# Optimization experiments

Measured on AMD Instinct MI355X. Metric: run time of the kernel, lower is better.

The kernel has to match this reference:

```python
import jax, jax.numpy as jnp
import numpy as np

B, S, E, H = 8, 512, 1024, 16
Dh = E // H
MAX_LEN = 512


def setup_inputs() -> dict:
    key = jax.random.key(0)
    ks = jax.random.split(key, 16)
    std = 1.0 / np.sqrt(E)
    inp = {
        "query": jax.random.normal(ks[0], (B, S, E), jnp.float32),
        "key": jax.random.normal(ks[1], (B, S, E), jnp.float32),
        "value": jax.random.normal(ks[2], (B, S, E), jnp.float32),
        "Wq": jax.random.normal(ks[3], (E, E), jnp.float32) * std,
        "bq": jax.random.normal(ks[4], (E,), jnp.float32) * std,
        "Wk": jax.random.normal(ks[5], (E, E), jnp.float32) * std,
        "bk": jax.random.normal(ks[6], (E,), jnp.float32) * std,
        "Wv": jax.random.normal(ks[7], (E, E), jnp.float32) * std,
        "bv": jax.random.normal(ks[8], (E,), jnp.float32) * std,
        "Wo": jax.random.normal(ks[9], (E, E), jnp.float32) * std,
        "bo": jax.random.normal(ks[10], (E,), jnp.float32) * std,
        "pos": jax.random.normal(ks[11], (MAX_LEN, 1, E), jnp.float32),
    }
    return inp


def reference(query, key, value, Wq, bq, Wk, bk, Wv, bv, Wo, bo, pos):
    b, sq, e = query.shape
    s = min(sq, key.shape[1])  # target_seq_length (static)
    scale = np.sqrt(Dh).astype(np.float32)
    pe = pos[:s, 0, :][None]  # [1, s, E] broadcast over batch
    q = query[:, :s] @ Wq.T + bq + pe
    k = key[:, :s] @ Wk.T + bk + pe
    v = value[:, :s] @ Wv.T + bv + pe
    # [b, s, H, Dh]
    q = q.reshape(b, s, H, Dh)
    k = k.reshape(b, s, H, Dh)
    v = v.reshape(b, s, H, Dh)
    scores = jnp.einsum("bqhd,bkhd->bhqk", q, k) / scale
    attn = jax.nn.softmax(scores, axis=-1)
    wv = jnp.einsum("bhqk,bkhd->bqhd", attn, v).reshape(b, s, e)
    return wv @ Wo.T + bo
```

## Files before the change

### kernel.cpp

```cpp
#include <hip/hip_runtime.h>
#include <hip/hip_bf16.h>

typedef __attribute__((ext_vector_type(8))) short bfx8;
typedef __attribute__((ext_vector_type(4))) short bfx4;
typedef __attribute__((ext_vector_type(4))) float fx4;

static __device__ __forceinline__ short f2bf(float f) {
  union { float f; unsigned u; } v; v.f = f;
  unsigned r = v.u + 0x7fffu + ((v.u >> 16) & 1u);
  return (short)(r >> 16);
}

static __device__ __forceinline__ void gld16(const void* g, void* l) {
  __builtin_amdgcn_global_load_lds(
      (const __attribute__((address_space(1))) void*)g,
      (__attribute__((address_space(3))) void*)l, 16, 0, 0);
}

constexpr int Bz = 8, Sq = 512, Em = 1024, Hn = 16, Dh = 64;
constexpr int Mrows = Bz * Sq;
constexpr size_t NE = (size_t)Mrows * Em;
constexpr size_t WE = (size_t)Em * Em;
constexpr int NT = Em / 64;

__global__ __launch_bounds__(256) void convert_kernel(
    const float* __restrict__ q, const float* __restrict__ k,
    const float* __restrict__ v,
    const float* __restrict__ Wq, const float* __restrict__ Wk,
    const float* __restrict__ Wv, const float* __restrict__ Wo,
    short* __restrict__ qx, short* __restrict__ kx, short* __restrict__ vx,
    short* __restrict__ wqb, short* __restrict__ wkb,
    short* __restrict__ wvb, short* __restrict__ wob)
{
  const size_t c = (size_t)blockIdx.x * 256 + threadIdx.x;
  constexpr size_t CI = NE / 8;
  constexpr size_t CW = WE / 8;
  const float* src; short* dst; size_t off;
  if (c < 3 * CI) {
    const int sgi = (int)(c / CI);
    src = sgi == 0 ? q : sgi == 1 ? k : v;
    dst = sgi == 0 ? qx : sgi == 1 ? kx : vx;
    off = (c - (size_t)sgi * CI) * 8;
  } else {
    const size_t w = c - 3 * CI;
    const int sgi = (int)(w / CW);
    src = sgi == 0 ? Wq : sgi == 1 ? Wk : sgi == 2 ? Wv : Wo;
    dst = sgi == 0 ? wqb : sgi == 1 ? wkb : sgi == 2 ? wvb : wob;
    off = (w - (size_t)sgi * CW) * 8;
  }
  fx4 a = *(const fx4*)(src + off);
  fx4 b = *(const fx4*)(src + off + 4);
  bfx8 o = { f2bf(a[0]), f2bf(a[1]), f2bf(a[2]), f2bf(a[3]),
             f2bf(b[0]), f2bf(b[1]), f2bf(b[2]), f2bf(b[3]) };
  *(bfx8*)(dst + off) = o;
}

__global__ __launch_bounds__(512, 2) void gemm_qkv_bf16(
    const short* __restrict__ qx, const short* __restrict__ kx,
    const short* __restrict__ vx,
    const short* __restrict__ Wqb, const short* __restrict__ Wkb,
    const short* __restrict__ Wvb,
    const float* __restrict__ bq, const float* __restrict__ bk,
    const float* __restrict__ bv,
    const float* __restrict__ pos,
    short* __restrict__ qb, short* __restrict__ kb, short* __restrict__ vb)
{
  __shared__ short SM[65536];

  const int z = blockIdx.z;
  const short* X = (z == 0) ? qx : (z == 1) ? kx : vx;
  const short* W = (z == 0) ? Wqb : (z == 1) ? Wkb : Wvb;
  const float* bias = (z == 0) ? bq : (z == 1) ? bk : bv;
  short* dst = (z == 0) ? qb : (z == 1) ? kb : vb;

  const int t0b = blockIdx.x * 256;
  const int f0 = blockIdx.y * 256;
  const int t = threadIdx.x, lane = t & 63, wave = t >> 6;
  const int wr = wave >> 2;
  const int wn = wave & 3;
  const int fr = lane & 15, fq = lane >> 4;

  const int srow = t >> 3;
  const int scc = (t & 7) ^ (srow & 7);
  const int sdst = wave * 512;

  const int sw0 = (fq ^ (fr & 7)) * 8;
  const int sw1 = ((4 + fq) ^ (fr & 7)) * 8;

  auto stageA = [&](int hh, int ktn, int pn) {
    const short* s = W + (size_t)(f0 + hh * 128 + srow) * Em + ktn * 64 + scc * 8;
    short* d = SM + pn * 32768 + hh * 8192 + sdst;
    gld16(s, d);
    gld16(s + (size_t)64 * Em, d + 4096);
  };
  auto stageB = [&](int hh, int ktn, int pn) {
    const short* s = X + (size_t)(t0b + hh * 128 + srow) * Em + ktn * 64 + scc * 8;
    short* d = SM + pn * 32768 + 16384 + hh * 8192 + sdst;
    gld16(s, d);
    gld16(s + (size_t)64 * Em, d + 4096);
  };

  fx4 acc[8][4] = {};

  stageA(0, 0, 0); stageA(1, 0, 0); stageB(0, 0, 0); stageB(1, 0, 0);
  __builtin_amdgcn_sched_barrier(0);
  asm volatile("s_waitcnt vmcnt(0)");
  __builtin_amdgcn_sched_barrier(0);
  __builtin_amdgcn_s_barrier();

  for (int kt = 0; kt < NT; ++kt) {
    const int p = kt & 1, pn = p ^ 1;
    const bool pre = (kt + 1 < NT);
    const short* Ab = SM + p * 32768 + wr * 8192;
    const short* Bb = SM + p * 32768 + 16384 + (wn >> 1) * 8192 + (wn & 1) * 4096;

    bfx8 bf[4][2];
#pragma unroll
    for (int q = 0; q < 4; ++q) {
      if (q == 0) {
#pragma unroll
        for (int cg = 0; cg < 4; ++cg) {
          bf[cg][0] = *(const bfx8*)&Bb[(cg * 16 + fr) * 64 + sw0];
          bf[cg][1] = *(const bfx8*)&Bb[(cg * 16 + fr) * 64 + sw1];
        }
      }
      bfx8 af[2][2];
#pragma unroll
      for (int rr2 = 0; rr2 < 2; ++rr2) {
        const int row = (q * 2 + rr2) * 16 + fr;
        af[rr2][0] = *(const bfx8*)&Ab[row * 64 + sw0];
        af[rr2][1] = *(const bfx8*)&Ab[row * 64 + sw1];
      }
      if (q == 0 && pre) { stageA(0, kt + 1, pn); stageA(1, kt + 1, pn); }
      if (q == 1 && pre) { stageB(0, kt + 1, pn); stageB(1, kt + 1, pn); }

      __builtin_amdgcn_sched_barrier(0);
      __builtin_amdgcn_s_barrier();
      __builtin_amdgcn_sched_barrier(0);

      __builtin_amdgcn_s_setprio(1);
#pragma unroll
      for (int rr2 = 0; rr2 < 2; ++rr2)
#pragma unroll
        for (int cg = 0; cg < 4; ++cg) {
          acc[q * 2 + rr2][cg] = __builtin_amdgcn_mfma_f32_16x16x32_bf16(
              af[rr2][0], bf[cg][0], acc[q * 2 + rr2][cg], 0, 0, 0);
          acc[q * 2 + rr2][cg] = __builtin_amdgcn_mfma_f32_16x16x32_bf16(
              af[rr2][1], bf[cg][1], acc[q * 2 + rr2][cg], 0, 0, 0);
        }
      __builtin_amdgcn_s_setprio(0);
      __builtin_amdgcn_sched_barrier(0);

      if (q == 3 && pre) {
        asm volatile("s_waitcnt vmcnt(0)");
        __builtin_amdgcn_sched_barrier(0);
      }
      __builtin_amdgcn_s_barrier();
    }
  }

  const int b = t0b >> 9;
  if (z < 2) {
#pragma unroll
    for (int fp = 0; fp < 2; ++fp) {
      if (fp) __syncthreads();
      if (wr == fp) {
#pragma unroll
        for (int rg = 0; rg < 8; ++rg) {
          const int nloc = rg * 16 + fq * 4;
          const int nng = f0 + fp * 128 + nloc;
          const fx4 bb = *(const fx4*)&bias[nng];
#pragma unroll
          for (int cg = 0; cg < 4; ++cg) {
            const int token = wn * 64 + cg * 16 + fr;
            const int s = (t0b + token) & (Sq - 1);
            const fx4 pe = *(const fx4*)&pos[(size_t)s * Em + nng];
            const fx4 a = acc[rg][cg];
            bfx4 o = { f2bf(a[0] + bb[0] + pe[0]), f2bf(a[1] + bb[1] + pe[1]),
                       f2bf(a[2] + bb[2] + pe[2]), f2bf(a[3] + bb[3] + pe[3]) };
            *(bfx4*)&SM[token * 136 + nloc] = o;
          }
        }
      }
      __syncthreads();
#pragma unroll
      for (int it = 0; it < 8; ++it) {
        const int flat = it * 512 + t;
        const int token = flat >> 4, ch = flat & 15;
        bfx8 val = *(const bfx8*)&SM[token * 136 + ch * 8];
        const int nng = f0 + fp * 128 + ch * 8;
        const int h = nng >> 6, d = nng & 63;
        const int s = (t0b + token) & (Sq - 1);
        *(bfx8*)&dst[(((size_t)b * Hn + h) * Sq + s) * Dh + d] = val;
      }
    }
  } else {
#pragma unroll
    for (int fp = 0; fp < 2; ++fp) {
      if (fp) __syncthreads();
      if (wr == fp) {
#pragma unroll
        for (int rg = 0; rg < 8; ++rg) {
          const int nloc = rg * 16 + fq * 4;
          const int nng = f0 + fp * 128 + nloc;
          const fx4 bb = *(const fx4*)&bias[nng];
#pragma unroll
          for (int cg = 0; cg < 4; ++cg) {
            const int token = wn * 64 + cg * 16 + fr;
            const int s = (t0b + token) & (Sq - 1);
            const fx4 pe = *(const fx4*)&pos[(size_t)s * Em + nng];
            const fx4 a = acc[rg][cg];
#pragma unroll
            for (int i = 0; i < 4; ++i)
              SM[(nloc + i) * 264 + token] = f2bf(a[i] + bb[i] + pe[i]);
          }
        }
      }
      __syncthreads();
      const int s0 = t0b & (Sq - 1);
#pragma unroll
      for (int it = 0; it < 8; ++it) {
        const int flat = it * 512 + t;
        const int row = flat >> 5, ch = flat & 31;
        bfx8 val = *(const bfx8*)&SM[row * 264 + ch * 8];
        const int nng = f0 + fp * 128 + row;
        const int h = nng >> 6, d = nng & 63;
        *(bfx8*)&dst[(((size_t)b * Hn + h) * Dh + d) * Sq + s0 + ch * 8] = val;
      }
    }
  }
}

constexpr int LDP = 136;

__global__ __launch_bounds__(256, 4) void gemm_out_bf16(
    const short* __restrict__ wv, const short* __restrict__ Wob,
    const float* __restrict__ bo, float* __restrict__ out)
{
  __shared__ short SMo[2 * 8192];
  short* As = SMo;
  short* Bs = SMo + 8192;

  const int m0 = blockIdx.x * 128;
  const int n0 = blockIdx.y * 128;
  const int t = threadIdx.x, lane = t & 63, wave = t >> 6;
  const int wr = wave >> 1, wc = wave & 1;
  const int fr = lane & 15, fq = lane >> 4;

  const int trow = t >> 3;
  const int scol = ((t & 7) ^ (trow & 7)) * 8;
  const short* gW = Wob + (size_t)(n0 + trow) * Em + scol;
  const short* gX = wv + (size_t)(m0 + trow) * Em + scol;
  short* lA = As + wave * 512;
  short* lB = Bs + wave * 512;

  const int sw0 = ((fq ^ (fr & 7)) * 8);
  const int sw1 = (((4 + fq) ^ (fr & 7)) * 8);

  fx4 acc[4][4] = {};

  for (int k0 = 0; k0 < Em; k0 += 64) {
#pragma unroll
    for (int r = 0; r < 4; ++r) {
      gld16(gW + (size_t)(32 * r) * Em + k0, lA + r * 2048);
      gld16(gX + (size_t)(32 * r) * Em + k0, lB + r * 2048);
    }
    __syncthreads();

#pragma unroll
    for (int ks = 0; ks < 2; ++ks) {
      const int sw = ks ? sw1 : sw0;
      bfx8 af[4], bf[4];
#pragma unroll
      for (int u = 0; u < 4; ++u)
        af[u] = *(const bfx8*)&As[(wr * 64 + u * 16 + fr) * 64 + sw];
#pragma unroll
      for (int v = 0; v < 4; ++v)
        bf[v] = *(const bfx8*)&Bs[(wc * 64 + v * 16 + fr) * 64 + sw];
#pragma unroll
      for (int u = 0; u < 4; ++u)
#pragma unroll
        for (int v = 0; v < 4; ++v)
          acc[u][v] = __builtin_amdgcn_mfma_f32_16x16x32_bf16(af[u], bf[v], acc[u][v], 0, 0, 0);
    }
    __syncthreads();
  }

#pragma unroll
  for (int u = 0; u < 4; ++u) {
    const int nn = n0 + wr * 64 + u * 16 + fq * 4;
    const fx4 bb = *(const fx4*)&bo[nn];
#pragma unroll
    for (int v = 0; v < 4; ++v) {
      const int m = m0 + wc * 64 + v * 16 + fr;
      fx4 val = acc[u][v];
      val[0] += bb[0]; val[1] += bb[1]; val[2] += bb[2]; val[3] += bb[3];
      *(fx4*)&out[(size_t)m * Em + nn] = val;
    }
  }
}

constexpr int KVB = 64, LDK = 72;

__global__ __launch_bounds__(512) void attn_kernel(
    const short* __restrict__ qb, const short* __restrict__ kb,
    const short* __restrict__ vb, short* __restrict__ wv)
{
  __shared__ short Ks[KVB * LDK];
  __shared__ short Vt[Dh * LDK];
  __shared__ short Ps[8][16 * LDK];

  const int bh = blockIdx.x;
  const int qt = blockIdx.y;
  const int t = threadIdx.x, lane = t & 63, wave = t >> 6;
  const int fr = lane & 15, fq = lane >> 4;

  const size_t base = (size_t)bh * Sq * Dh;
  const int q0 = qt * 128 + wave * 16;

  bfx8 qf[2];
  {
    const short* qp = qb + base + (size_t)(q0 + fr) * Dh;
    qf[0] = *(const bfx8*)(qp + fq * 8);
    qf[1] = *(const bfx8*)(qp + 32 + fq * 8);
  }

  const int kr = t >> 3, kc = (t & 7) * 8;
  const short* kbp = kb + base + (size_t)kr * Dh + kc;
  const short* vbp = vb + base + (size_t)kr * Sq + kc;

  {
    bfx8 k0 = *(const bfx8*)kbp;
    bfx8 v0 = *(const bfx8*)vbp;
    *(bfx8*)&Ks[kr * LDK + kc] = k0;
    *(bfx8*)&Vt[kr * LDK + kc] = v0;
  }
  __syncthreads();

  float mrow[4] = { -1e30f, -1e30f, -1e30f, -1e30f };
  float lrow[4] = { 0.f, 0.f, 0.f, 0.f };
  fx4 oacc[4] = {};

  for (int kv0 = 0; kv0 < Sq; kv0 += KVB) {
    const bool more = (kv0 + KVB) < Sq;
    bfx8 nk0, nv0;
    if (more) {
      nk0 = *(const bfx8*)(kbp + (size_t)(kv0 + KVB) * Dh);
      nv0 = *(const bfx8*)(vbp + kv0 + KVB);
    }

    fx4 sa[4] = {};
    __builtin_amdgcn_s_setprio(1);
#pragma unroll
    for (int nf = 0; nf < 4; ++nf) {
#pragma unroll
      for (int ks = 0; ks < 2; ++ks) {
        bfx8 kf = *(const bfx8*)&Ks[(nf * 16 + fr) * LDK + ks * 32 + fq * 8];
        sa[nf] = __builtin_amdgcn_mfma_f32_16x16x32_bf16(qf[ks], kf, sa[nf], 0, 0, 0);
      }
    }
    __builtin_amdgcn_s_setprio(0);

#pragma unroll
    for (int i = 0; i < 4; ++i) {
      float mx = fmaxf(fmaxf(sa[0][i], sa[1][i]), fmaxf(sa[2][i], sa[3][i]));
      mx = fmaxf(mx, __shfl_xor(mx, 1));
      mx = fmaxf(mx, __shfl_xor(mx, 2));
      mx = fmaxf(mx, __shfl_xor(mx, 4));
      mx = fmaxf(mx, __shfl_xor(mx, 8));
      mx *= 0.125f;
      if (mx > mrow[i] + 8.f) {
        const float alpha = __expf(mrow[i] - mx);
        mrow[i] = mx;
        lrow[i] *= alpha;
#pragma unroll
        for (int df = 0; df < 4; ++df) oacc[df][i] *= alpha;
      }
      float rs = 0.f;
#pragma unroll
      for (int nf = 0; nf < 4; ++nf) {
        const float p = __expf(sa[nf][i] * 0.125f - mrow[i]);
        rs += p;
        Ps[wave][(fq * 4 + i) * LDK + nf * 16 + fr] = f2bf(p);
      }
      rs += __shfl_xor(rs, 1);
      rs += __shfl_xor(rs, 2);
      rs += __shfl_xor(rs, 4);
      rs += __shfl_xor(rs, 8);
      lrow[i] += rs;
    }

    bfx8 pf[2];
    pf[0] = *(const bfx8*)&Ps[wave][fr * LDK + fq * 8];
    pf[1] = *(const bfx8*)&Ps[wave][fr * LDK + 32 + fq * 8];
    __builtin_amdgcn_s_setprio(1);
#pragma unroll
    for (int df = 0; df < 4; ++df) {
#pragma unroll
      for (int ks = 0; ks < 2; ++ks) {
        bfx8 vf = *(const bfx8*)&Vt[(df * 16 + fr) * LDK + ks * 32 + fq * 8];
        oacc[df] = __builtin_amdgcn_mfma_f32_16x16x32_bf16(pf[ks], vf, oacc[df], 0, 0, 0);
      }
    }
    __builtin_amdgcn_s_setprio(0);
    __syncthreads();

    if (more) {
      *(bfx8*)&Ks[kr * LDK + kc] = nk0;
      *(bfx8*)&Vt[kr * LDK + kc] = nv0;
      __syncthreads();
    }
  }

  const int b = bh >> 4, h = bh & 15;
#pragma unroll
  for (int df = 0; df < 4; ++df) {
    const int d = df * 16 + fr;
#pragma unroll
    for (int i = 0; i < 4; ++i) {
      const int qrow = q0 + fq * 4 + i;
      const float o = oacc[df][i] / lrow[i];
      wv[((size_t)b * Sq + qrow) * Em + h * Dh + d] = f2bf(o);
    }
  }
}

extern "C" void kernel_launch(void* const* d_in, const int* in_sizes, int n_in,
                              void* d_out, int out_size, void* d_ws, size_t ws_size,
                              hipStream_t stream) {
  (void)in_sizes; (void)n_in; (void)out_size; (void)ws_size;
  const float* query = (const float*)d_in[0];
  const float* key   = (const float*)d_in[1];
  const float* value = (const float*)d_in[2];
  const float* Wq = (const float*)d_in[3];
  const float* bq = (const float*)d_in[4];
  const float* Wk = (const float*)d_in[5];
  const float* bk = (const float*)d_in[6];
  const float* Wv = (const float*)d_in[7];
  const float* bv = (const float*)d_in[8];
  const float* Wo = (const float*)d_in[9];
  const float* bo = (const float*)d_in[10];
  const float* pos = (const float*)d_in[11];

  short* qx = (short*)d_ws;
  short* kx = qx + NE;
  short* vx = kx + NE;
  short* Wqb = vx + NE;
  short* Wkb = Wqb + WE;
  short* Wvb = Wkb + WE;
  short* Wob = Wvb + WE;
  short* qb = Wob + WE;
  short* wv = qx;
  short* kb = (short*)d_out;
  short* vb = kb + NE;

  convert_kernel<<<dim3(8192), 256, 0, stream>>>(
      query, key, value, Wq, Wk, Wv, Wo, qx, kx, vx, Wqb, Wkb, Wvb, Wob);
  gemm_qkv_bf16<<<dim3(Mrows / 256, Em / 256, 3), 512, 0, stream>>>(
      qx, kx, vx, Wqb, Wkb, Wvb, bq, bk, bv, pos, qb, kb, vb);
  attn_kernel<<<dim3(Bz * Hn, Sq / 128), 512, 0, stream>>>(qb, kb, vb, wv);
  gemm_out_bf16<<<dim3(Mrows / 128, Em / 128), 256, 0, stream>>>(
      wv, Wob, bo, (float*)d_out);
}
```

Baseline: 109.7 us.

## Restructure QKV projection GEMM to 4-stage BK=32 software pipeline

Replaces the double-buffered BK=64 main loop of the QKV projection GEMM with a four-slot ring of BK=32 tiles, prefetching three K-steps ahead. Partial vmcnt waits replace full drains, so global loads stay in flight across iterations, and each step now uses one barrier pair instead of several sub-phases. The LDS swizzle changes to suit 32-wide rows. In exchange there are twice as many K iterations, each with two barriers, and the hard-coded vmcnt counts must match the number of issued loads exactly.

```diff
diff --git a/kernel.cpp b/kernel.cpp
--- a/kernel.cpp
+++ b/kernel.cpp
@@ -21,7 +21,6 @@
 constexpr int Mrows = Bz * Sq;
 constexpr size_t NE = (size_t)Mrows * Em;
 constexpr size_t WE = (size_t)Em * Em;
-constexpr int NT = Em / 64;
 
 __global__ __launch_bounds__(256) void convert_kernel(
     const float* __restrict__ q, const float* __restrict__ k,
@@ -80,83 +79,58 @@
   const int wn = wave & 3;
   const int fr = lane & 15, fq = lane >> 4;
 
-  const int srow = t >> 3;
-  const int scc = (t & 7) ^ (srow & 7);
-  const int sdst = wave * 512;
-
-  const int sw0 = (fq ^ (fr & 7)) * 8;
-  const int sw1 = ((4 + fq) ^ (fr & 7)) * 8;
-
-  auto stageA = [&](int hh, int ktn, int pn) {
-    const short* s = W + (size_t)(f0 + hh * 128 + srow) * Em + ktn * 64 + scc * 8;
-    short* d = SM + pn * 32768 + hh * 8192 + sdst;
-    gld16(s, d);
-    gld16(s + (size_t)64 * Em, d + 4096);
+  const int srow = t >> 2;
+  const int scol = ((t & 3) ^ ((t >> 3) & 3)) * 8;
+  const short* gA = W + (size_t)(f0 + srow) * Em + scol;
+  const short* gB = X + (size_t)(t0b + srow) * Em + scol;
+  const int ldst = wave * 512;
+
+  auto stage = [&](int ktn) {
+    short* sl = SM + (ktn & 3) * 16384;
+    const int ko = ktn * 32;
+#pragma unroll
+    for (int g = 0; g < 2; ++g) {
+      gld16(gA + (size_t)(g * 128) * Em + ko, sl + g * 4096 + ldst);
+      gld16(gB + (size_t)(g * 128) * Em + ko, sl + 8192 + g * 4096 + ldst);
+    }
   };
-  auto stageB = [&](int hh, int ktn, int pn) {
-    const short* s = X + (size_t)(t0b + hh * 128 + srow) * Em + ktn * 64 + scc * 8;
-    short* d = SM + pn * 32768 + 16384 + hh * 8192 + sdst;
-    gld16(s, d);
-    gld16(s + (size_t)64 * Em, d + 4096);
-  };
+
+  const int csw = (fq ^ ((fr >> 1) & 3)) * 8;
 
   fx4 acc[8][4] = {};
 
-  stageA(0, 0, 0); stageA(1, 0, 0); stageB(0, 0, 0); stageB(1, 0, 0);
-  __builtin_amdgcn_sched_barrier(0);
-  asm volatile("s_waitcnt vmcnt(0)");
-  __builtin_amdgcn_sched_barrier(0);
-  __builtin_amdgcn_s_barrier();
-
-  for (int kt = 0; kt < NT; ++kt) {
-    const int p = kt & 1, pn = p ^ 1;
-    const bool pre = (kt + 1 < NT);
-    const short* Ab = SM + p * 32768 + wr * 8192;
-    const short* Bb = SM + p * 32768 + 16384 + (wn >> 1) * 8192 + (wn & 1) * 4096;
-
-    bfx8 bf[4][2];
-#pragma unroll
-    for (int q = 0; q < 4; ++q) {
-      if (q == 0) {
-#pragma unroll
-        for (int cg = 0; cg < 4; ++cg) {
-          bf[cg][0] = *(const bfx8*)&Bb[(cg * 16 + fr) * 64 + sw0];
-          bf[cg][1] = *(const bfx8*)&Bb[(cg * 16 + fr) * 64 + sw1];
-        }
-      }
-      bfx8 af[2][2];
-#pragma unroll
-      for (int rr2 = 0; rr2 < 2; ++rr2) {
-        const int row = (q * 2 + rr2) * 16 + fr;
-        af[rr2][0] = *(const bfx8*)&Ab[row * 64 + sw0];
-        af[rr2][1] = *(const bfx8*)&Ab[row * 64 + sw1];
-      }
-      if (q == 0 && pre) { stageA(0, kt + 1, pn); stageA(1, kt + 1, pn); }
-      if (q == 1 && pre) { stageB(0, kt + 1, pn); stageB(1, kt + 1, pn); }
-
-      __builtin_amdgcn_sched_barrier(0);
-      __builtin_amdgcn_s_barrier();
-      __builtin_amdgcn_sched_barrier(0);
-
-      __builtin_amdgcn_s_setprio(1);
-#pragma unroll
-      for (int rr2 = 0; rr2 < 2; ++rr2)
-#pragma unroll
-        for (int cg = 0; cg < 4; ++cg) {
-          acc[q * 2 + rr2][cg] = __builtin_amdgcn_mfma_f32_16x16x32_bf16(
-              af[rr2][0], bf[cg][0], acc[q * 2 + rr2][cg], 0, 0, 0);
-          acc[q * 2 + rr2][cg] = __builtin_amdgcn_mfma_f32_16x16x32_bf16(
-              af[rr2][1], bf[cg][1], acc[q * 2 + rr2][cg], 0, 0, 0);
-        }
-      __builtin_amdgcn_s_setprio(0);
-      __builtin_amdgcn_sched_barrier(0);
-
-      if (q == 3 && pre) {
-        asm volatile("s_waitcnt vmcnt(0)");
-        __builtin_amdgcn_sched_barrier(0);
-      }
-      __builtin_amdgcn_s_barrier();
-    }
+  stage(0); stage(1); stage(2);
+  for (int kt = 0; kt < 32; ++kt) {
+    if (kt < 29) stage(kt + 3);
+    __builtin_amdgcn_sched_barrier(0);
+    if (kt < 29)       asm volatile("s_waitcnt vmcnt(12)");
+    else if (kt == 29) asm volatile("s_waitcnt vmcnt(8)");
+    else if (kt == 30) asm volatile("s_waitcnt vmcnt(4)");
+    else               asm volatile("s_waitcnt vmcnt(0)");
+    __builtin_amdgcn_sched_barrier(0);
+    __builtin_amdgcn_s_barrier();
+
+    const short* slA = SM + (kt & 3) * 16384;
+    const short* slB = slA + 8192;
+
+    bfx8 af[8], bf[4];
+#pragma unroll
+    for (int rg = 0; rg < 8; ++rg)
+      af[rg] = *(const bfx8*)&slA[(wr * 128 + rg * 16 + fr) * 32 + csw];
+#pragma unroll
+    for (int cg = 0; cg < 4; ++cg)
+      bf[cg] = *(const bfx8*)&slB[(wn * 64 + cg * 16 + fr) * 32 + csw];
+
+    __builtin_amdgcn_s_setprio(1);
+#pragma unroll
+    for (int rg = 0; rg < 8; ++rg)
+#pragma unroll
+      for (int cg = 0; cg < 4; ++cg)
+        acc[rg][cg] = __builtin_amdgcn_mfma_f32_16x16x32_bf16(
+            af[rg], bf[cg], acc[rg][cg], 0, 0, 0);
+    __builtin_amdgcn_s_setprio(0);
+    __builtin_amdgcn_sched_barrier(0);
+    __builtin_amdgcn_s_barrier();
   }
 
   const int b = t0b >> 9;
```

New measurement: 111.8 us. Within noise of the previous version (+1.9%).
